# Optimization experiments

Measured on AMD Instinct MI355X. Metric: run time of the kernel, lower is better.

## Reference

```python
import jax, jax.numpy as jnp
import numpy as np

B, T, C = 2, 2048, 1024
H = 16
D = C // H  # head_dim = 64


def setup_inputs() -> dict:
    key = jax.random.key(0)
    k1, k2, k3, k4, k5 = jax.random.split(key, 5)
    s = 0.02
    return {
        "x": jax.random.normal(k1, (B, T, C), dtype=jnp.float32),
        "w_qkv": jax.random.normal(k2, (C, 3 * C), dtype=jnp.float32) * s,
        "b_qkv": jnp.zeros((3 * C,), dtype=jnp.float32),
        "w_proj": jax.random.normal(k3, (C, C), dtype=jnp.float32) * s,
        "b_proj": jnp.zeros((C,), dtype=jnp.float32),
    }


def reference(x, w_qkv, b_qkv, w_proj, b_proj):
    b, t, c = x.shape
    qkv = x @ w_qkv + b_qkv                      # [B,T,3C]
    q, k, v = jnp.split(qkv, 3, axis=-1)
    # [B,T,C] -> [B,H,T,D]
    q = q.reshape(b, t, H, D).transpose(0, 2, 1, 3)
    k = k.reshape(b, t, H, D).transpose(0, 2, 1, 3)
    v = v.reshape(b, t, H, D).transpose(0, 2, 1, 3)
    att = jnp.einsum("bhqd,bhkd->bhqk", q, k) / jnp.sqrt(jnp.float32(D))
    causal = jnp.tril(jnp.ones((t, t), dtype=bool))  # True where allowed
    att = jnp.where(causal, att, -jnp.inf)
    att = jax.nn.softmax(att, axis=-1)
    out = jnp.einsum("bhqk,bhkd->bhqd", att, v)      # [B,H,T,D]
    out = out.transpose(0, 2, 1, 3).reshape(b, t, c)
    return out @ w_proj + b_proj
```

## Files before the change

kernel.cpp:

```cpp
#include <hip/hip_runtime.h>
#include <hip/hip_bf16.h>
#include <math.h>
#include <stdint.h>

#define B_ 2
#define T_ 2048
#define C_ 1024
#define H_ 16
#define D_ 64

typedef __attribute__((ext_vector_type(8))) short bf16x8;
typedef __attribute__((ext_vector_type(4))) float f32x4;

__device__ inline short f2bf(float f) {
  __hip_bfloat16 h = __float2bfloat16(f);
  return *(short*)&h;
}

__device__ inline void async16(const void* g, void* l) {
  __builtin_amdgcn_global_load_lds(
      (const __attribute__((address_space(1))) uint32_t*)g,
      (__attribute__((address_space(3))) uint32_t*)l, 16, 0, 0);
}


__global__ __launch_bounds__(256) void prep(
    const float* __restrict__ X, const float* __restrict__ Wq,
    const float* __restrict__ Wp, short* __restrict__ Xb,
    short* __restrict__ Wqt, short* __restrict__ Wpt) {
  const int tid = threadIdx.x;
  const int blk = blockIdx.x;
  __shared__ short Ts[64][68];

  if (blk < 512) {
    const int g = tid >> 3;
    const int sub = tid & 7;
    const int sc = sub >> 1;
    const int e4 = (sub & 1) * 4;
#pragma unroll
    for (int pass = 0; pass < 8; ++pass) {
      const int m = blk * 8 + pass;
      float4 v = *(const float4*)(X + (size_t)m * C_ + tid * 4);
      const int xv = (m >> 1) & 3;
      short o[4] = {f2bf(v.x), f2bf(v.y), f2bf(v.z), f2bf(v.w)};
      *(uint2*)(Xb + (size_t)m * C_ + g * 32 + ((sc ^ xv) << 3) + e4) =
          *(uint2*)o;
    }
    return;
  }

  const float* W;
  short* Wt;
  int N, n0, k0;
  if (blk < 1280) {
    int i = blk - 512;
    W = Wq; Wt = Wqt; N = 3 * C_;
    n0 = (i % 48) * 64; k0 = (i / 48) * 64;
  } else {
    int i = blk - 1280;
    W = Wp; Wt = Wpt; N = C_;
    n0 = (i & 15) * 64; k0 = (i >> 4) * 64;
  }
  {
    int r = tid >> 2, c0 = (tid & 3) * 16;
    const float* src = W + (size_t)(k0 + r) * N + n0 + c0;
#pragma unroll
    for (int u = 0; u < 16; u += 4) {
      float4 v = *(const float4*)(src + u);
      Ts[r][c0 + u + 0] = f2bf(v.x);
      Ts[r][c0 + u + 1] = f2bf(v.y);
      Ts[r][c0 + u + 2] = f2bf(v.z);
      Ts[r][c0 + u + 3] = f2bf(v.w);
    }
  }
  __syncthreads();
#pragma unroll
  for (int p = 0; p < 2; ++p) {
    int n = (tid >> 3) + p * 32;
    int kc = tid & 7;
    int xv = ((n0 + n) >> 1) & 3;
    int ka = kc * 8;
    int dk = (ka & ~31) | ((((ka >> 3) & 3) ^ xv) << 3);
    short tmp[8];
#pragma unroll
    for (int u = 0; u < 8; ++u) tmp[u] = Ts[ka + u][n];
    *(uint4*)(Wt + (size_t)(n0 + n) * 1024 + k0 + dk) = *(uint4*)tmp;
  }
}

template <int N, int BN, bool QKV>
__global__ __launch_bounds__(256, 2) void gemm_mfma(
    const short* __restrict__ A, const short* __restrict__ Bt,
    const float* __restrict__ bias, short* __restrict__ Qp,
    short* __restrict__ Kp, short* __restrict__ Vp, float* __restrict__ Cout) {
  constexpr int NJ = BN / 32;
  constexpr int BI = BN * 32;
  constexpr int LPS = 2 + BN / 64;
  const int tid = threadIdx.x;
  const int wave = tid >> 6, lane = tid & 63;
  const int quad = lane >> 4, l16 = lane & 15;
  const int wm = wave >> 1, wn = wave & 1;

  const int f = blockIdx.x;
  const int xcd = f & 7, r = f >> 3;
  const int lby = r >> 3, lbx = r & 7;
  const int by = (xcd >> 1) * 8 + lby;
  const int bx = (xcd & 1) * 8 + lbx;
  const int m0 = by * 128, n0 = bx * BN;

  __shared__ short As[4][4096];
  __shared__ short Bs[4][BI];

  const int srow = tid >> 2, skc = tid & 3;
  const size_t arow0 = (size_t)(m0 + srow) * 1024 + skc * 8;
  const size_t brow0 = (size_t)(n0 + srow) * 1024 + skc * 8;

  f32x4 acc[4][NJ] = {};

  const int xi = quad ^ ((l16 >> 1) & 3);
  int aoff[4], boff[NJ];
#pragma unroll
  for (int i = 0; i < 4; ++i) aoff[i] = (wm * 64 + i * 16 + l16) * 32 + xi * 8;
#pragma unroll
  for (int j = 0; j < NJ; ++j)
    boff[j] = (wn * (BN / 2) + j * 16 + l16) * 32 + xi * 8;

  auto stage = [&](int t) {
    const int s = t & 3;
    const size_t kf = (size_t)t * 32;
    async16(A + arow0 + kf, &As[s][tid * 8]);
    async16(A + arow0 + (size_t)64 * 1024 + kf, &As[s][2048 + tid * 8]);
#pragma unroll
    for (int seg = 0; seg < BN / 64; ++seg)
      async16(Bt + brow0 + (size_t)(seg * 64) * 1024 + kf,
              &Bs[s][seg * 2048 + tid * 8]);
  };

  stage(0);
  stage(1);
  for (int t = 0; t < 32; ++t) {
    const int s = t & 3;
    if (t + 2 < 32) {
      stage(t + 2);
      if constexpr (BN == 192)
        __asm__ volatile("s_waitcnt vmcnt(10)" ::: "memory");
      else
        __asm__ volatile("s_waitcnt vmcnt(6)" ::: "memory");
    } else if (t + 1 < 32) {
      if constexpr (BN == 192)
        __asm__ volatile("s_waitcnt vmcnt(5)" ::: "memory");
      else
        __asm__ volatile("s_waitcnt vmcnt(3)" ::: "memory");
    } else {
      __asm__ volatile("s_waitcnt vmcnt(0)" ::: "memory");
    }
    __builtin_amdgcn_s_barrier();

    bf16x8 af[4], bfr[NJ];
#pragma unroll
    for (int i = 0; i < 4; ++i) af[i] = *(const bf16x8*)&As[s][aoff[i]];
#pragma unroll
    for (int j = 0; j < NJ; ++j) bfr[j] = *(const bf16x8*)&Bs[s][boff[j]];
#pragma unroll
    for (int i = 0; i < 4; ++i)
#pragma unroll
      for (int j = 0; j < NJ; ++j)
        acc[i][j] = __builtin_amdgcn_mfma_f32_16x16x32_bf16(
            af[i], bfr[j], acc[i][j], 0, 0, 0);
  }

  float bj[NJ];
#pragma unroll
  for (int j = 0; j < NJ; ++j) bj[j] = bias[n0 + wn * (BN / 2) + j * 16 + l16];

  if (QKV) {
#pragma unroll
    for (int i = 0; i < 4; ++i) {
#pragma unroll
      for (int reg = 0; reg < 4; ++reg) {
        int m = m0 + wm * 64 + i * 16 + quad * 4 + reg;
        int b = m >> 11, t = m & (T_ - 1);
#pragma unroll
        for (int j = 0; j < NJ; ++j) {
          int n = n0 + wn * (BN / 2) + j * 16 + l16;
          float v = acc[i][j][reg] + bj[j];
          int sel = n >> 10, cc = n & (C_ - 1);
          int hh = cc >> 6, d = cc & 63;
          size_t base = (size_t)(b * H_ + hh) * 131072 + (size_t)(t >> 6) * 4096;
          if (sel == 0) {
            Qp[base + (d >> 3) * 512 + (t & 63) * 8 + (d & 7)] =
                f2bf(v * 0.18033688011112042f);
          } else if (sel == 1) {
            Kp[base + (d >> 3) * 512 + (t & 63) * 8 + (d & 7)] = f2bf(v);
          } else {
            Vp[base + ((t & 63) >> 3) * 512 + d * 8 + (t & 7)] = f2bf(v);
          }
        }
      }
    }
  } else {
#pragma unroll
    for (int i = 0; i < 4; ++i) {
#pragma unroll
      for (int reg = 0; reg < 4; ++reg) {
        int m = m0 + wm * 64 + i * 16 + quad * 4 + reg;
#pragma unroll
        for (int j = 0; j < NJ; ++j) {
          int n = n0 + wn * (BN / 2) + j * 16 + l16;
          Cout[(size_t)m * N + n] = acc[i][j][reg] + bj[j];
        }
      }
    }
  }
}

__global__ __launch_bounds__(256, 2) void attn_kernel(
    const short* __restrict__ Qt, const short* __restrict__ Kt,
    const short* __restrict__ Vt, short* __restrict__ attb) {
  const int tid = threadIdx.x;
  const int wave = tid >> 6, lane = tid & 63;
  const int quad = lane >> 4, l16 = lane & 15;

  const int blk = blockIdx.x;
  const int bh = blk & 31;
  const int i = blk >> 5;
  const int pj = (i < 8) ? (15 - i) : (i - 8);
  const int NT = 2 * pj + 2;
  const int h = bh & 15, b = bh >> 4;

  const short* Qg = Qt + (size_t)bh * 131072;
  const short* Kg = Kt + (size_t)bh * 131072;
  const short* Vg = Vt + (size_t)bh * 131072;

  __shared__ short Ks[2][4096];
  __shared__ short Vs[2][4096];
  __shared__ short Ps[2][4096];

  const int rowl = 16 * wave + l16;

  bf16x8 bq[2][2];
#pragma unroll
  for (int g = 0; g < 2; ++g)
#pragma unroll
    for (int f = 0; f < 2; ++f)
      bq[g][f] = *(const bf16x8*)(Qg +
                 (size_t)((2 * pj + g) * 8 + 4 * f + quad) * 512 + rowl * 8);

  async16(Kg + tid * 8, &Ks[0][tid * 8]);
  async16(Kg + 2048 + tid * 8, &Ks[0][2048 + tid * 8]);
  async16(Vg + tid * 8, &Vs[0][tid * 8]);
  async16(Vg + 2048 + tid * 8, &Vs[0][2048 + tid * 8]);

  f32x4 oacc[4][2] = {};
  float lsum[2] = {0.f, 0.f};

  auto stage_next = [&](int kt) {
    const int dst = (kt + 1) & 1;
    const short* kp = Kg + (size_t)(kt + 1) * 4096;
    const short* vp = Vg + (size_t)(kt + 1) * 4096;
    async16(kp + tid * 8, &Ks[dst][tid * 8]);
    async16(kp + 2048 + tid * 8, &Ks[dst][2048 + tid * 8]);
    async16(vp + tid * 8, &Vs[dst][tid * 8]);
    async16(vp + 2048 + tid * 8, &Vs[dst][2048 + tid * 8]);
  };

  auto qkt2 = [&](int buf, f32x4 (&sacc)[4][2]) {
    __builtin_amdgcn_s_setprio(1);
#pragma unroll
    for (int c = 0; c < 4; ++c) {
#pragma unroll
      for (int f = 0; f < 2; ++f) {
        bf16x8 ak =
            *(const bf16x8*)&Ks[buf][((4 * f + quad) * 64 + 16 * c + l16) * 8];
        sacc[c][0] = __builtin_amdgcn_mfma_f32_16x16x32_bf16(
            ak, bq[0][f], sacc[c][0], 0, 0, 0);
        sacc[c][1] = __builtin_amdgcn_mfma_f32_16x16x32_bf16(
            ak, bq[1][f], sacc[c][1], 0, 0, 0);
      }
    }
    __builtin_amdgcn_s_setprio(0);
  };

  auto smax = [&](f32x4 (&sacc)[4][2], int g, bool mask) {
#pragma unroll
    for (int c = 0; c < 4; ++c) {
      short4 pk;
#pragma unroll
      for (int reg = 0; reg < 4; ++reg) {
        int keyl = 16 * c + 4 * quad + reg;
        float p = (mask && keyl > rowl)
                      ? 0.f
                      : __builtin_amdgcn_exp2f(sacc[c][g][reg]);
        lsum[g] += p;
        ((short*)&pk)[reg] = f2bf(p);
      }
      *(short4*)&Ps[g][(2 * c + (quad >> 1)) * 512 + rowl * 8 + (quad & 1) * 4] =
          pk;
    }
  };

  auto pv2 = [&](int buf) {
    __asm__ volatile("s_waitcnt lgkmcnt(0)" ::: "memory");
    bf16x8 ap[2][2];
#pragma unroll
    for (int f = 0; f < 2; ++f) {
      ap[0][f] = *(const bf16x8*)&Ps[0][(4 * f + quad) * 512 + rowl * 8];
      ap[1][f] = *(const bf16x8*)&Ps[1][(4 * f + quad) * 512 + rowl * 8];
    }
    __builtin_amdgcn_s_setprio(1);
#pragma unroll
    for (int n = 0; n < 4; ++n) {
#pragma unroll
      for (int f = 0; f < 2; ++f) {
        bf16x8 bv =
            *(const bf16x8*)&Vs[buf][((4 * f + quad) * 64 + 16 * n + l16) * 8];
        oacc[n][0] = __builtin_amdgcn_mfma_f32_16x16x32_bf16(
            ap[0][f], bv, oacc[n][0], 0, 0, 0);
        oacc[n][1] = __builtin_amdgcn_mfma_f32_16x16x32_bf16(
            ap[1][f], bv, oacc[n][1], 0, 0, 0);
      }
    }
    __builtin_amdgcn_s_setprio(0);
  };

  for (int kt = 0; kt < NT - 2; ++kt) {
    const int buf = kt & 1;
    __syncthreads();
    stage_next(kt);
    f32x4 sacc[4][2] = {};
    qkt2(buf, sacc);
    smax(sacc, 0, false);
    smax(sacc, 1, false);
    pv2(buf);
  }
  {
    const int kt = NT - 2, buf = kt & 1;
    __syncthreads();
    stage_next(kt);
    f32x4 sacc[4][2] = {};
    qkt2(buf, sacc);
    smax(sacc, 0, true);
    smax(sacc, 1, false);
    pv2(buf);
  }
  {
    const int buf = (NT - 1) & 1;
    __syncthreads();
    f32x4 sacc1[4] = {};
    __builtin_amdgcn_s_setprio(1);
#pragma unroll
    for (int c = 0; c < 4; ++c)
#pragma unroll
      for (int f = 0; f < 2; ++f) {
        bf16x8 ak =
            *(const bf16x8*)&Ks[buf][((4 * f + quad) * 64 + 16 * c + l16) * 8];
        sacc1[c] = __builtin_amdgcn_mfma_f32_16x16x32_bf16(
            ak, bq[1][f], sacc1[c], 0, 0, 0);
      }
    __builtin_amdgcn_s_setprio(0);
#pragma unroll
    for (int c = 0; c < 4; ++c) {
      short4 pk;
#pragma unroll
      for (int reg = 0; reg < 4; ++reg) {
        int keyl = 16 * c + 4 * quad + reg;
        float p = (keyl > rowl) ? 0.f : __builtin_amdgcn_exp2f(sacc1[c][reg]);
        lsum[1] += p;
        ((short*)&pk)[reg] = f2bf(p);
      }
      *(short4*)&Ps[1][(2 * c + (quad >> 1)) * 512 + rowl * 8 + (quad & 1) * 4] =
          pk;
    }
    __asm__ volatile("s_waitcnt lgkmcnt(0)" ::: "memory");
    bf16x8 ap1[2];
#pragma unroll
    for (int f = 0; f < 2; ++f)
      ap1[f] = *(const bf16x8*)&Ps[1][(4 * f + quad) * 512 + rowl * 8];
    __builtin_amdgcn_s_setprio(1);
#pragma unroll
    for (int n = 0; n < 4; ++n)
#pragma unroll
      for (int f = 0; f < 2; ++f) {
        bf16x8 bv =
            *(const bf16x8*)&Vs[buf][((4 * f + quad) * 64 + 16 * n + l16) * 8];
        oacc[n][1] = __builtin_amdgcn_mfma_f32_16x16x32_bf16(
            ap1[f], bv, oacc[n][1], 0, 0, 0);
      }
    __builtin_amdgcn_s_setprio(0);
  }

#pragma unroll
  for (int g = 0; g < 2; ++g) {
    float ls = lsum[g];
    ls += __shfl_xor(ls, 16);
    ls += __shfl_xor(ls, 32);
    float linv[4];
#pragma unroll
    for (int reg = 0; reg < 4; ++reg)
      linv[reg] = 1.0f / __shfl(ls, 4 * quad + reg, 64);
#pragma unroll
    for (int reg = 0; reg < 4; ++reg) {
      const int row = (2 * pj + g) * 64 + 16 * wave + 4 * quad + reg;
      const int m = b * T_ + row;
      const int xv = (m >> 1) & 3;
#pragma unroll
      for (int n = 0; n < 4; ++n) {
        int c = h * 64 + 16 * n + l16;
        int cs = (c & ~31) | ((((c >> 3) & 3) ^ xv) << 3) | (c & 7);
        attb[(size_t)m * C_ + cs] = f2bf(oacc[n][g][reg] * linv[reg]);
      }
    }
  }
}

extern "C" void kernel_launch(void* const* d_in, const int* in_sizes, int n_in,
                              void* d_out, int out_size, void* d_ws, size_t ws_size,
                              hipStream_t stream) {
  const float* x      = (const float*)d_in[0];
  const float* w_qkv  = (const float*)d_in[1];
  const float* b_qkv  = (const float*)d_in[2];
  const float* w_proj = (const float*)d_in[3];
  const float* b_proj = (const float*)d_in[4];
  float* out = (float*)d_out;

  const size_t per = (size_t)B_ * H_ * T_ * D_;
  short* Qp   = (short*)d_ws;
  short* Kp   = Qp + per;
  short* Vp   = Kp + per;
  short* attb = Vp + per;
  short* xb   = attb + per;
  short* wqt  = xb + per;
  short* wpt  = wqt + (size_t)3 * C_ * C_;

  prep<<<1536, 256, 0, stream>>>(x, w_qkv, w_proj, xb, wqt, wpt);

  gemm_mfma<3 * C_, 192, true><<<dim3(512), 256, 0, stream>>>(
      xb, wqt, b_qkv, Qp, Kp, Vp, nullptr);

  attn_kernel<<<dim3(512), 256, 0, stream>>>(Qp, Kp, Vp, attb);

  gemm_mfma<C_, 64, false><<<dim3(512), 256, 0, stream>>>(
      attb, wpt, b_proj, nullptr, nullptr, nullptr, out);
}
```

Measured before the change: 176.0 us.

## Double GEMM M-tile to 256 with 512-thread blocks and MFMA priority boost

Both GEMM kernels now use 512-thread blocks covering 256 rows of A instead of 128, and launch half as many blocks. The async global-to-LDS loads and per-wave vmcnt waits are rebalanced so that only the first four waves load the leftover B rows. MFMA sections are wrapped in s_setprio to favour matrix issue. The aim is more reuse of each B tile and fewer redundant loads. In exchange, LDS use per block grows, occupancy drops to one block per CU, and the grid now just fills the CUs once.

Measured after the change: 177.7 us. About the same (+1.0%).

```diff
diff --git a/kernel.cpp b/kernel.cpp
--- a/kernel.cpp
+++ b/kernel.cpp
@@ -89,13 +89,12 @@
 }
 
 template <int N, int BN, bool QKV>
-__global__ __launch_bounds__(256, 2) void gemm_mfma(
+__global__ __launch_bounds__(512, 1) void gemm_mfma(
     const short* __restrict__ A, const short* __restrict__ Bt,
     const float* __restrict__ bias, short* __restrict__ Qp,
     short* __restrict__ Kp, short* __restrict__ Vp, float* __restrict__ Cout) {
   constexpr int NJ = BN / 32;
   constexpr int BI = BN * 32;
-  constexpr int LPS = 2 + BN / 64;
   const int tid = threadIdx.x;
   const int wave = tid >> 6, lane = tid & 63;
   const int quad = lane >> 4, l16 = lane & 15;
@@ -104,16 +103,17 @@
   const int f = blockIdx.x;
   const int xcd = f & 7, r = f >> 3;
   const int lby = r >> 3, lbx = r & 7;
-  const int by = (xcd >> 1) * 8 + lby;
+  const int by = (xcd >> 1) * 4 + lby;
   const int bx = (xcd & 1) * 8 + lbx;
-  const int m0 = by * 128, n0 = bx * BN;
-
-  __shared__ short As[4][4096];
+  const int m0 = by * 256, n0 = bx * BN;
+
+  __shared__ short As[4][8192];
   __shared__ short Bs[4][BI];
 
   const int srow = tid >> 2, skc = tid & 3;
   const size_t arow0 = (size_t)(m0 + srow) * 1024 + skc * 8;
   const size_t brow0 = (size_t)(n0 + srow) * 1024 + skc * 8;
+  const size_t brow2 = (size_t)(n0 + 128 + srow) * 1024 + skc * 8;
 
   f32x4 acc[4][NJ] = {};
 
@@ -129,11 +129,15 @@
     const int s = t & 3;
     const size_t kf = (size_t)t * 32;
     async16(A + arow0 + kf, &As[s][tid * 8]);
-    async16(A + arow0 + (size_t)64 * 1024 + kf, &As[s][2048 + tid * 8]);
-#pragma unroll
-    for (int seg = 0; seg < BN / 64; ++seg)
-      async16(Bt + brow0 + (size_t)(seg * 64) * 1024 + kf,
-              &Bs[s][seg * 2048 + tid * 8]);
+    async16(A + arow0 + (size_t)128 * 1024 + kf, &As[s][4096 + tid * 8]);
+    if constexpr (BN == 192) {
+      async16(Bt + brow0 + kf, &Bs[s][tid * 8]);
+      if (wave < 4)
+        async16(Bt + brow2 + kf, &Bs[s][4096 + tid * 8]);
+    } else {
+      if (wave < 4)
+        async16(Bt + brow0 + kf, &Bs[s][tid * 8]);
+    }
   };
 
   stage(0);
@@ -142,15 +146,21 @@
     const int s = t & 3;
     if (t + 2 < 32) {
       stage(t + 2);
-      if constexpr (BN == 192)
-        __asm__ volatile("s_waitcnt vmcnt(10)" ::: "memory");
-      else
-        __asm__ volatile("s_waitcnt vmcnt(6)" ::: "memory");
+      if constexpr (BN == 192) {
+        if (wave < 4) __asm__ volatile("s_waitcnt vmcnt(8)" ::: "memory");
+        else          __asm__ volatile("s_waitcnt vmcnt(6)" ::: "memory");
+      } else {
+        if (wave < 4) __asm__ volatile("s_waitcnt vmcnt(6)" ::: "memory");
+        else          __asm__ volatile("s_waitcnt vmcnt(4)" ::: "memory");
+      }
     } else if (t + 1 < 32) {
-      if constexpr (BN == 192)
-        __asm__ volatile("s_waitcnt vmcnt(5)" ::: "memory");
-      else
-        __asm__ volatile("s_waitcnt vmcnt(3)" ::: "memory");
+      if constexpr (BN == 192) {
+        if (wave < 4) __asm__ volatile("s_waitcnt vmcnt(4)" ::: "memory");
+        else          __asm__ volatile("s_waitcnt vmcnt(3)" ::: "memory");
+      } else {
+        if (wave < 4) __asm__ volatile("s_waitcnt vmcnt(3)" ::: "memory");
+        else          __asm__ volatile("s_waitcnt vmcnt(2)" ::: "memory");
+      }
     } else {
       __asm__ volatile("s_waitcnt vmcnt(0)" ::: "memory");
     }
@@ -161,12 +171,14 @@
     for (int i = 0; i < 4; ++i) af[i] = *(const bf16x8*)&As[s][aoff[i]];
 #pragma unroll
     for (int j = 0; j < NJ; ++j) bfr[j] = *(const bf16x8*)&Bs[s][boff[j]];
+    __builtin_amdgcn_s_setprio(1);
 #pragma unroll
     for (int i = 0; i < 4; ++i)
 #pragma unroll
       for (int j = 0; j < NJ; ++j)
         acc[i][j] = __builtin_amdgcn_mfma_f32_16x16x32_bf16(
             af[i], bfr[j], acc[i][j], 0, 0, 0);
+    __builtin_amdgcn_s_setprio(0);
   }
 
   float bj[NJ];
@@ -434,11 +446,11 @@
 
   prep<<<1536, 256, 0, stream>>>(x, w_qkv, w_proj, xb, wqt, wpt);
 
-  gemm_mfma<3 * C_, 192, true><<<dim3(512), 256, 0, stream>>>(
+  gemm_mfma<3 * C_, 192, true><<<dim3(256), 512, 0, stream>>>(
       xb, wqt, b_qkv, Qp, Kp, Vp, nullptr);
 
   attn_kernel<<<dim3(512), 256, 0, stream>>>(Qp, Kp, Vp, attb);
 
-  gemm_mfma<C_, 64, false><<<dim3(512), 256, 0, stream>>>(
+  gemm_mfma<C_, 64, false><<<dim3(256), 512, 0, stream>>>(
       attb, wpt, b_proj, nullptr, nullptr, nullptr, out);
 }
```
